# Performance work log

Measured on AMD Instinct MI355X. Metric: run time of the kernel, lower is better.

## Reference

```python
import jax, jax.numpy as jnp
import numpy as np

B, N, D, H = 2, 1024, 512, 16
DH = D // H  # d_head = 32
NEG_INF = -1e9
LN_EPS = 1e-5


def setup_inputs() -> dict:
    key = jax.random.key(0)
    ks = jax.random.split(key, 12)
    x = jax.random.normal(ks[0], (B, N, D), dtype=jnp.float32)
    pdist = jax.random.uniform(ks[1], (B, N, N), dtype=jnp.float32)
    angle = jax.random.normal(ks[2], (B, N, N, 2), dtype=jnp.float32)
    adj = jax.random.uniform(ks[3], (B, N, N), dtype=jnp.float32)
    mask = jnp.zeros((B, 1, 1, N), dtype=bool)
    # parameters
    gamma_p = jnp.ones((H,), dtype=jnp.float32)
    gamma_adj = jnp.ones((H,), dtype=jnp.float32)
    w_bias = jax.random.normal(ks[4], (H, 2), dtype=jnp.float32) / np.sqrt(2.0)   # Linear(2,H).weight
    att_w = jax.random.normal(ks[5], (3 * H * DH, D), dtype=jnp.float32) / np.sqrt(D)  # Linear(D,3HDh).weight
    ff_w = jax.random.normal(ks[6], (D, H * DH), dtype=jnp.float32) / np.sqrt(H * DH)  # Linear(HDh,D).weight
    ff_b = jnp.zeros((D,), dtype=jnp.float32)
    ln_w = jnp.ones((D,), dtype=jnp.float32)
    ln_b = jnp.zeros((D,), dtype=jnp.float32)
    return dict(x=x, pdist=pdist, angle=angle, adj=adj, mask=mask,
                gamma_p=gamma_p, gamma_adj=gamma_adj, w_bias=w_bias,
                att_w=att_w, ff_w=ff_w, ff_b=ff_b, ln_w=ln_w, ln_b=ln_b)


def reference(x, pdist, angle, adj, mask, gamma_p, gamma_adj, w_bias,
              att_w, ff_w, ff_b, ln_w, ln_b):
    bsz, n_atoms, _ = x.shape
    # QKV projection
    qkv = x @ att_w.T                              # [B,N,3*H*DH]
    wq, wk, wv = jnp.split(qkv, 3, axis=-1)
    wq = wq.reshape(bsz, n_atoms, H, DH)
    wk = wk.reshape(bsz, n_atoms, H, DH)
    wv = wv.reshape(bsz, n_atoms, H, DH)
    # scores with additive biases
    score = jnp.einsum('bihd,bjhd->bhij', wq, wk) / jnp.sqrt(jnp.float32(DH))
    score = score - gamma_p[None, :, None, None] * pdist[:, None]
    angle_bias = jnp.einsum('bijc,hc->bhij', angle, w_bias)
    score = score + angle_bias
    score = score + gamma_adj[None, :, None, None] * adj[:, None]
    score = jnp.where(mask, NEG_INF, score)
    prob = jax.nn.softmax(score, axis=-1)          # [B,H,N,N]
    att_vec = jnp.einsum('bhij,bjhd->bihd', prob, wv).reshape(bsz, n_atoms, H * DH)
    ff_out = att_vec @ ff_w.T + ff_b               # [B,N,D]
    y = x + ff_out
    mu = jnp.mean(y, axis=-1, keepdims=True)
    var = jnp.mean(jnp.square(y - mu), axis=-1, keepdims=True)
    return (y - mu) / jnp.sqrt(var + LN_EPS) * ln_w + ln_b
```

## Files before the change

### kernel.cpp

```cpp
#include <hip/hip_runtime.h>
#include <hip/hip_bf16.h>
#include <stdint.h>

#define DEVI __device__ __forceinline__

typedef __attribute__((ext_vector_type(4))) float f32x4;
typedef __attribute__((ext_vector_type(16))) float f32x16;
typedef __attribute__((ext_vector_type(8))) short bf16x8;

constexpr int nB = 2, nN = 1024, nD = 512, nH = 16, nDH = 32;

DEVI unsigned short f2bf(float x) {
  unsigned u = __float_as_uint(x);
  return (unsigned short)((u + 0x7fffu + ((u >> 16) & 1u)) >> 16);
}
DEVI float bf2f(unsigned short s) { return __uint_as_float(((unsigned)s) << 16); }
DEVI unsigned pk2(float lo, float hi_) {
  return (unsigned)f2bf(lo) | ((unsigned)f2bf(hi_) << 16);
}
DEVI float bperm(int srclane, float v) {
  return __int_as_float(__builtin_amdgcn_ds_bpermute(srclane << 2, __float_as_int(v)));
}
DEVI void gload16(const void* g, void* l) {
  __builtin_amdgcn_global_load_lds((const __attribute__((address_space(1))) void*)g,
                                   (__attribute__((address_space(3))) void*)l, 16, 0, 0);
}

__global__ __launch_bounds__(256) void cvt_fw(const float* __restrict__ fw,
                                              unsigned short* __restrict__ fwb) {
  int i = blockIdx.x * 256 + threadIdx.x;
  float4 v = reinterpret_cast<const float4*>(fw)[i];
  ushort4 o;
  o.x = f2bf(v.x); o.y = f2bf(v.y); o.z = f2bf(v.z); o.w = f2bf(v.w);
  reinterpret_cast<ushort4*>(fwb)[i] = o;
}

__global__ __launch_bounds__(256, 2) void qkv_gemm(const float* __restrict__ x,
                                                   const float* __restrict__ aw,
                                                   unsigned short* __restrict__ q,
                                                   unsigned short* __restrict__ kmat,
                                                   unsigned short* __restrict__ vtt) {
  __shared__ __align__(16) unsigned short sA[2][64 * 32];
  __shared__ __align__(16) unsigned short sB[2][128 * 32];
  const int tid = threadIdx.x, wid = tid >> 6, lane = tid & 63;
  const int wr = wid >> 1, wc = wid & 1;
  const long rowA = (long)blockIdx.x * 64;
  const long rowB = (long)blockIdx.y * 128;

  f32x4 acc[2][4];
#pragma unroll
  for (int mm = 0; mm < 2; ++mm)
#pragma unroll
    for (int nn = 0; nn < 4; ++nn)
#pragma unroll
      for (int r = 0; r < 4; ++r) acc[mm][nn][r] = 0.f;

  union PK { unsigned u[4]; bf16x8 v; };

  auto stage = [&](int t, int pb) {
    const int k0 = t * 32;
    {
      const float* src = x + (rowA + (tid >> 2)) * 512 + k0 + (tid & 3) * 8;
      float4 v0 = *reinterpret_cast<const float4*>(src);
      float4 v1 = *reinterpret_cast<const float4*>(src + 4);
      PK p;
      p.u[0] = pk2(v0.x, v0.y); p.u[1] = pk2(v0.z, v0.w);
      p.u[2] = pk2(v1.x, v1.y); p.u[3] = pk2(v1.z, v1.w);
      *reinterpret_cast<bf16x8*>(&sA[pb][tid * 8]) = p.v;
    }
    {
      const float* src = aw + (rowB + (tid >> 1)) * 512 + k0 + (tid & 1) * 16;
      float4 w0 = *reinterpret_cast<const float4*>(src);
      float4 w1 = *reinterpret_cast<const float4*>(src + 4);
      float4 w2 = *reinterpret_cast<const float4*>(src + 8);
      float4 w3 = *reinterpret_cast<const float4*>(src + 12);
      PK p0, p1;
      p0.u[0] = pk2(w0.x, w0.y); p0.u[1] = pk2(w0.z, w0.w);
      p0.u[2] = pk2(w1.x, w1.y); p0.u[3] = pk2(w1.z, w1.w);
      p1.u[0] = pk2(w2.x, w2.y); p1.u[1] = pk2(w2.z, w2.w);
      p1.u[2] = pk2(w3.x, w3.y); p1.u[3] = pk2(w3.z, w3.w);
      *reinterpret_cast<bf16x8*>(&sB[pb][tid * 16]) = p0.v;
      *reinterpret_cast<bf16x8*>(&sB[pb][tid * 16 + 8]) = p1.v;
    }
  };
  auto comp = [&](int pb) {
    const int kg = (lane >> 4) * 8, rlo = lane & 15;
    bf16x8 af[2], bfv[4];
#pragma unroll
    for (int mm = 0; mm < 2; ++mm)
      af[mm] = *reinterpret_cast<const bf16x8*>(&sA[pb][(32 * wr + 16 * mm + rlo) * 32 + kg]);
#pragma unroll
    for (int nn = 0; nn < 4; ++nn)
      bfv[nn] = *reinterpret_cast<const bf16x8*>(&sB[pb][(64 * wc + 16 * nn + rlo) * 32 + kg]);
#pragma unroll
    for (int mm = 0; mm < 2; ++mm)
#pragma unroll
      for (int nn = 0; nn < 4; ++nn)
        acc[mm][nn] = __builtin_amdgcn_mfma_f32_16x16x32_bf16(af[mm], bfv[nn],
                                                              acc[mm][nn], 0, 0, 0);
  };

  stage(0, 0);
  __syncthreads();
  for (int t = 0; t < 16; t += 2) {
    if (t + 1 < 16) stage(t + 1, 1);
    comp(0);
    __syncthreads();
    if (t + 2 < 16) stage(t + 2, 0);
    comp(1);
    __syncthreads();
  }

#pragma unroll
  for (int mm = 0; mm < 2; ++mm)
#pragma unroll
    for (int nn = 0; nn < 4; ++nn)
#pragma unroll
      for (int r = 0; r < 4; ++r) {
        float v = acc[mm][nn][r];
        int row = (int)rowA + 32 * wr + 16 * mm + (lane >> 4) * 4 + r;
        int col = (int)rowB + 64 * wc + 16 * nn + (lane & 15);
        int s = col >> 9, rem = col & 511;
        int h = rem >> 5, d = rem & 31;
        int b = row >> 10, n = row & 1023;
        if (s == 0) {
          q[((long)(b * nH + h) * nN + n) * nDH + d] = f2bf(v * 0.1767766952966369f);
        } else if (s == 1) {
          kmat[((long)(b * nH + h) * nN + n) * nDH + d] = f2bf(v);
        } else {
          vtt[((long)(b * nH + h) * 32 + (n >> 5)) * 1024 + d * 32 + (n & 31)] = f2bf(v);
        }
      }
}

__global__ __launch_bounds__(1024, 4) void attn_kernel(
    const unsigned short* __restrict__ qm, const unsigned short* __restrict__ km,
    const unsigned short* __restrict__ vtt,
    const float* __restrict__ pdist, const float* __restrict__ angle,
    const float* __restrict__ adj, const unsigned char* __restrict__ mask,
    const float* __restrict__ gamma_p, const float* __restrict__ gamma_adj,
    const float* __restrict__ w_bias,
    unsigned short* __restrict__ po, float* __restrict__ pm, float* __restrict__ pl) {
  const int b = blockIdx.x >> 5, it = blockIdx.x & 31;
  const int jc = blockIdx.y;
  const int tid = threadIdx.x, wid = tid >> 6, lane = tid & 63;
  const int h = wid;
  const int li = lane & 31, hi = lane >> 5;
  const int ibase = it * 32;

  __shared__ __align__(16) float s_pd[2][1024], s_adj[2][1024];
  __shared__ __align__(16) float s_a0[2][1024], s_a1[2][1024];
  __shared__ __align__(16) float s_mk[1024];

  const float gp = gamma_p[h], ga = gamma_adj[h];
  const float wb0 = w_bias[2 * h], wb1 = w_bias[2 * h + 1];

  const unsigned short* qb = qm + ((long)(b * nH + h) * nN + ibase) * nDH;
  const bf16x8 qf0 = *reinterpret_cast<const bf16x8*>(qb + li * 32 + hi * 8);
  const bf16x8 qf1 = *reinterpret_cast<const bf16x8*>(qb + li * 32 + 16 + hi * 8);

  f32x16 o;
#pragma unroll
  for (int r = 0; r < 16; ++r) o[r] = 0.f;
  float mrun = -INFINITY, lrun = 0.f;

  auto stage = [&](int s, int pb) {
    const int jbase = (jc * 4 + s) * 32;
    if (tid < 512) {
      int r = (tid >> 3) & 31, c = tid & 7;
      const float* src = (tid < 256 ? pdist : adj) +
                         ((long)b * nN + ibase + r) * nN + jbase + c * 4;
      float4 v = *reinterpret_cast<const float4*>(src);
      float* dst = (tid < 256 ? s_pd[pb] : s_adj[pb]) + r * 32 + ((c ^ (r & 7)) << 2);
      *reinterpret_cast<float4*>(dst) = v;
    } else {
      int t2 = tid - 512;
      int r = t2 >> 4, p = t2 & 15;
      float4 v = *reinterpret_cast<const float4*>(
          angle + (((long)b * nN + ibase + r) * nN + jbase + p * 2) * 2);
      int off = r * 32 + (((p >> 1) ^ (r & 7)) << 2) + (p & 1) * 2;
      *reinterpret_cast<float2*>(s_a0[pb] + off) = make_float2(v.x, v.z);
      *reinterpret_cast<float2*>(s_a1[pb] + off) = make_float2(v.y, v.w);
    }
  };

  auto comp = [&](int s, int pb) {
    const int jt = jc * 4 + s, jbase = jt * 32;
    const unsigned short* kb = km + ((long)(b * nH + h) * nN + jbase) * nDH;
    bf16x8 kf0 = *reinterpret_cast<const bf16x8*>(kb + li * 32 + hi * 8);
    bf16x8 kf1 = *reinterpret_cast<const bf16x8*>(kb + li * 32 + 16 + hi * 8);
    const unsigned short* vb = vtt + ((long)(b * nH + h) * 32 + jt) * 1024;
    bf16x8 vf0 = *reinterpret_cast<const bf16x8*>(vb + li * 32 + hi * 8);
    bf16x8 vf1 = *reinterpret_cast<const bf16x8*>(vb + li * 32 + 16 + hi * 8);

    f32x16 sc;
#pragma unroll
    for (int r = 0; r < 16; ++r) sc[r] = 0.f;
    sc = __builtin_amdgcn_mfma_f32_32x32x16_bf16(kf0, qf0, sc, 0, 0, 0);
    sc = __builtin_amdgcn_mfma_f32_32x32x16_bf16(kf1, qf1, sc, 0, 0, 0);

    float sv[16];
    float tmax = -INFINITY;
#pragma unroll
    for (int g = 0; g < 4; ++g) {
      const int cs = (((2 * g + hi) ^ (li & 7)) << 2);
      f32x4 pdq = *reinterpret_cast<const f32x4*>(s_pd[pb] + li * 32 + cs);
      f32x4 adq = *reinterpret_cast<const f32x4*>(s_adj[pb] + li * 32 + cs);
      f32x4 a0q = *reinterpret_cast<const f32x4*>(s_a0[pb] + li * 32 + cs);
      f32x4 a1q = *reinterpret_cast<const f32x4*>(s_a1[pb] + li * 32 + cs);
      f32x4 mkq = *reinterpret_cast<const f32x4*>(s_mk + jbase + 8 * g + 4 * hi);
#pragma unroll
      for (int u = 0; u < 4; ++u) {
        float xv = sc[4 * g + u] - gp * pdq[u] + wb0 * a0q[u] + wb1 * a1q[u]
                   + ga * adq[u] + mkq[u];
        sv[4 * g + u] = xv;
        tmax = fmaxf(tmax, xv);
      }
    }
    tmax = fmaxf(tmax, __shfl_xor(tmax, 32));
    if (__any((int)(tmax > mrun + 8.f))) {
      float mnew = fmaxf(mrun, tmax);
      float alpha = __expf(mrun - mnew);
      lrun *= alpha;
#pragma unroll
      for (int r = 0; r < 16; ++r) o[r] *= bperm((r & 3) + 8 * (r >> 2) + 4 * hi, alpha);
      mrun = mnew;
    }
    float psum = 0.f;
#pragma unroll
    for (int r = 0; r < 16; ++r) { sv[r] = __expf(sv[r] - mrun); psum += sv[r]; }
    psum += __shfl_xor(psum, 32);
    lrun += psum;

    unsigned ow[8], rw[8];
#pragma unroll
    for (int t = 0; t < 8; ++t) ow[t] = pk2(sv[2 * t], sv[2 * t + 1]);
#pragma unroll
    for (int t = 0; t < 8; ++t) rw[t] = __shfl_xor(ow[t], 32);
    union U { unsigned u[4]; bf16x8 v; };
    U u0, u1;
    if (hi == 0) {
      u0.u[0] = ow[0]; u0.u[1] = ow[1]; u0.u[2] = rw[0]; u0.u[3] = rw[1];
      u1.u[0] = ow[4]; u1.u[1] = ow[5]; u1.u[2] = rw[4]; u1.u[3] = rw[5];
    } else {
      u0.u[0] = rw[2]; u0.u[1] = rw[3]; u0.u[2] = ow[2]; u0.u[3] = ow[3];
      u1.u[0] = rw[6]; u1.u[1] = rw[7]; u1.u[2] = ow[6]; u1.u[3] = ow[7];
    }

    o = __builtin_amdgcn_mfma_f32_32x32x16_bf16(u0.v, vf0, o, 0, 0, 0);
    o = __builtin_amdgcn_mfma_f32_32x32x16_bf16(u1.v, vf1, o, 0, 0, 0);
  };

  s_mk[tid] = mask[b * nN + tid] ? -1e9f : 0.f;
  stage(0, 0);
  __syncthreads();
  for (int s = 0; s < 4; s += 2) {
    if (s + 1 < 4) stage(s + 1, 1);
    comp(s, 0);
    __syncthreads();
    if (s + 2 < 4) stage(s + 2, 0);
    comp(s + 1, 1);
    __syncthreads();
  }

  const long task = (((long)(b * nH + h) * 32 + it) * 8 + jc);
  unsigned short* pob = po + task * 1024;
#pragma unroll
  for (int r = 0; r < 16; ++r) {
    const int irow = (r & 3) + 8 * (r >> 2) + 4 * hi;
    pob[irow * 32 + li] = f2bf(o[r]);
  }
  if (hi == 0) { pm[task * 32 + li] = mrun; pl[task * 32 + li] = lrun; }
}

__global__ __launch_bounds__(256) void merge_kernel(const unsigned short* __restrict__ po,
                                                    const float* __restrict__ pm,
                                                    const float* __restrict__ pl,
                                                    unsigned short* __restrict__ attb) {
  const int x = blockIdx.x;
  const int t = threadIdx.x;
  const int i = t >> 3, d4 = (t & 7) * 4;
  const long tb = (long)x * 8;
  float m[8], l[8];
#pragma unroll
  for (int c = 0; c < 8; ++c) { m[c] = pm[(tb + c) * 32 + i]; l[c] = pl[(tb + c) * 32 + i]; }
  float M = m[0];
#pragma unroll
  for (int c = 1; c < 8; ++c) M = fmaxf(M, m[c]);
  float L = 0.f, w[8];
#pragma unroll
  for (int c = 0; c < 8; ++c) { w[c] = __expf(m[c] - M); L += w[c] * l[c]; }
  float o0 = 0, o1 = 0, o2 = 0, o3 = 0;
#pragma unroll
  for (int c = 0; c < 8; ++c) {
    ushort4 v = *reinterpret_cast<const ushort4*>(po + (tb + c) * 1024 + i * 32 + d4);
    o0 += w[c] * bf2f(v.x); o1 += w[c] * bf2f(v.y);
    o2 += w[c] * bf2f(v.z); o3 += w[c] * bf2f(v.w);
  }
  const float inv = 1.f / L;
  const int b = x >> 9, hh = (x >> 5) & 15, it = x & 31;
  ushort4 ov;
  ov.x = f2bf(o0 * inv); ov.y = f2bf(o1 * inv);
  ov.z = f2bf(o2 * inv); ov.w = f2bf(o3 * inv);
  *reinterpret_cast<ushort4*>(attb + ((long)b * nN + it * 32 + i) * nD + hh * 32 + d4) = ov;
}

__global__ __launch_bounds__(512, 2) void ffln_kernel(const unsigned short* __restrict__ attb,
                                                      const unsigned short* __restrict__ fwb,
                                                      const float* __restrict__ x,
                                                      const float* __restrict__ ffb,
                                                      const float* __restrict__ lnw,
                                                      const float* __restrict__ lnb,
                                                      float* __restrict__ out) {
  __shared__ __align__(16) unsigned short sA[2][32 * 32];
  __shared__ __align__(16) unsigned short sB[2][512 * 32];
  __shared__ float rs_[32][4], rs2_[32][4];
  const int tid = threadIdx.x, wid = tid >> 6, lane = tid & 63;
  const int wr = wid >> 2, wc = wid & 3;
  const long rowA = (long)blockIdx.x * 32;

  f32x4 acc[8];
#pragma unroll
  for (int nn = 0; nn < 8; ++nn)
#pragma unroll
    for (int r = 0; r < 4; ++r) acc[nn][r] = 0.f;

  auto stage = [&](int t, int pb) {
    const int k0 = t * 32;
    if (tid < 128)
      gload16(&attb[(rowA + (tid >> 2)) * 512 + k0 + (tid & 3) * 8], &sA[pb][tid * 8]);
#pragma unroll
    for (int c = 0; c < 4; ++c) {
      int off = (tid + 512 * c) * 8;
      int r = off >> 5, s8 = off & 31;
      gload16(&fwb[(long)r * 512 + k0 + s8], &sB[pb][off]);
    }
  };
  auto comp = [&](int pb) {
    const int kg = (lane >> 4) * 8, rlo = lane & 15;
    bf16x8 af = *reinterpret_cast<const bf16x8*>(&sA[pb][(16 * wr + rlo) * 32 + kg]);
#pragma unroll
    for (int nn = 0; nn < 8; ++nn) {
      bf16x8 bfv = *reinterpret_cast<const bf16x8*>(&sB[pb][(128 * wc + 16 * nn + rlo) * 32 + kg]);
      acc[nn] = __builtin_amdgcn_mfma_f32_16x16x32_bf16(af, bfv, acc[nn], 0, 0, 0);
    }
  };

  stage(0, 0);
  __syncthreads();
  for (int t = 0; t < 16; t += 2) {
    if (t + 1 < 16) stage(t + 1, 1);
    comp(0);
    __syncthreads();
    if (t + 2 < 16) stage(t + 2, 0);
    comp(1);
    __syncthreads();
  }

  float colf[8], colw[8], colb[8];
#pragma unroll
  for (int nn = 0; nn < 8; ++nn) {
    int c = 128 * wc + 16 * nn + (lane & 15);
    colf[nn] = ffb[c]; colw[nn] = lnw[c]; colb[nn] = lnb[c];
  }
  float s[4], s2[4];
#pragma unroll
  for (int r = 0; r < 4; ++r) { s[r] = 0.f; s2[r] = 0.f; }
#pragma unroll
  for (int nn = 0; nn < 8; ++nn)
#pragma unroll
    for (int r = 0; r < 4; ++r) {
      long row = rowA + 16 * wr + 4 * (lane >> 4) + r;
      int c = 128 * wc + 16 * nn + (lane & 15);
      float y = acc[nn][r] + colf[nn] + x[row * 512 + c];
      acc[nn][r] = y;
      s[r] += y; s2[r] += y * y;
    }
#pragma unroll
  for (int off = 1; off < 16; off <<= 1)
#pragma unroll
    for (int r = 0; r < 4; ++r) {
      s[r] += __shfl_xor(s[r], off);
      s2[r] += __shfl_xor(s2[r], off);
    }
  if ((lane & 15) == 0) {
#pragma unroll
    for (int r = 0; r < 4; ++r) {
      int rowl = 16 * wr + 4 * (lane >> 4) + r;
      rs_[rowl][wc] = s[r];
      rs2_[rowl][wc] = s2[r];
    }
  }
  __syncthreads();
#pragma unroll
  for (int r = 0; r < 4; ++r) {
    int rowl = 16 * wr + 4 * (lane >> 4) + r;
    float S = rs_[rowl][0] + rs_[rowl][1] + rs_[rowl][2] + rs_[rowl][3];
    float S2 = rs2_[rowl][0] + rs2_[rowl][1] + rs2_[rowl][2] + rs2_[rowl][3];
    float mu = S * (1.f / 512.f);
    float var = S2 * (1.f / 512.f) - mu * mu;
    float rstd = rsqrtf(var + 1e-5f);
    long row = rowA + rowl;
#pragma unroll
    for (int nn = 0; nn < 8; ++nn) {
      int c = 128 * wc + 16 * nn + (lane & 15);
      out[row * 512 + c] = (acc[nn][r] - mu) * rstd * colw[nn] + colb[nn];
    }
  }
}

extern "C" void kernel_launch(void* const* d_in, const int* in_sizes, int n_in,
                              void* d_out, int out_size, void* d_ws, size_t ws_size,
                              hipStream_t stream) {
  const float* x         = (const float*)d_in[0];
  const float* pdist     = (const float*)d_in[1];
  const float* angle     = (const float*)d_in[2];
  const float* adj       = (const float*)d_in[3];
  const unsigned char* mask = (const unsigned char*)d_in[4];
  const float* gamma_p   = (const float*)d_in[5];
  const float* gamma_adj = (const float*)d_in[6];
  const float* w_bias    = (const float*)d_in[7];
  const float* att_w     = (const float*)d_in[8];
  const float* ff_w      = (const float*)d_in[9];
  const float* ff_b      = (const float*)d_in[10];
  const float* ln_w      = (const float*)d_in[11];
  const float* ln_b      = (const float*)d_in[12];
  float* out = (float*)d_out;

  char* ws = (char*)d_ws;
  unsigned short* qm   = (unsigned short*)(ws);
  unsigned short* km   = (unsigned short*)(ws + 0x200000);
  unsigned short* vtt  = (unsigned short*)(ws + 0x400000);
  unsigned short* po   = (unsigned short*)(ws + 0x600000);
  float*          pm   = (float*)(ws + 0x1600000);
  float*          pl   = (float*)(ws + 0x1700000);
  unsigned short* attb = (unsigned short*)(ws + 0x1800000);
  unsigned short* fwb  = (unsigned short*)(ws + 0x1A00000);

  hipLaunchKernelGGL(cvt_fw, dim3(256), dim3(256), 0, stream, ff_w, fwb);
  hipLaunchKernelGGL(qkv_gemm, dim3(32, 12), dim3(256), 0, stream,
                     x, att_w, qm, km, vtt);
  hipLaunchKernelGGL(attn_kernel, dim3(64, 8), dim3(1024), 0, stream,
                     qm, km, vtt, pdist, angle, adj, mask,
                     gamma_p, gamma_adj, w_bias, po, pm, pl);
  hipLaunchKernelGGL(merge_kernel, dim3(1024), dim3(256), 0, stream,
                     po, pm, pl, attb);
  hipLaunchKernelGGL(ffln_kernel, dim3(64), dim3(512), 0, stream,
                     attb, fwb, x, ff_b, ln_w, ln_b, out);
}
```

Baseline: 181.7 us.

## Use async global-to-LDS loads, exp2 softmax, and fewer key splits in attention

The attention kernel now stages pdist, adj and angle tiles with direct global_load_lds transfers and an XOR swizzle, replacing register round-trips, and keeps angle interleaved in a single buffer. The pipeline waits on vmcnt and raw barriers. The key dimension is split into 4 chunks of 8 tiles instead of 8 chunks of 4, which halves the partial results the merge kernel reads but also halves grid parallelism. Softmax switches to exp2 with log2e folded into the scale and bias coefficients, and bf16 packing uses the hardware packed-convert intrinsic.

```diff
diff --git a/kernel.cpp b/kernel.cpp
--- a/kernel.cpp
+++ b/kernel.cpp
@@ -9,14 +9,16 @@
 typedef __attribute__((ext_vector_type(8))) short bf16x8;
 
 constexpr int nB = 2, nN = 1024, nD = 512, nH = 16, nDH = 32;
+constexpr float L2E = 1.4426950408889634f;
 
 DEVI unsigned short f2bf(float x) {
   unsigned u = __float_as_uint(x);
   return (unsigned short)((u + 0x7fffu + ((u >> 16) & 1u)) >> 16);
 }
 DEVI float bf2f(unsigned short s) { return __uint_as_float(((unsigned)s) << 16); }
-DEVI unsigned pk2(float lo, float hi_) {
-  return (unsigned)f2bf(lo) | ((unsigned)f2bf(hi_) << 16);
+DEVI unsigned pkcvt(float lo, float hi_) {
+  __hip_bfloat162 h = __float22bfloat162_rn(make_float2(lo, hi_));
+  union { __hip_bfloat162 h; unsigned u; } c; c.h = h; return c.u;
 }
 DEVI float bperm(int srclane, float v) {
   return __int_as_float(__builtin_amdgcn_ds_bpermute(srclane << 2, __float_as_int(v)));
@@ -30,9 +32,9 @@
                                               unsigned short* __restrict__ fwb) {
   int i = blockIdx.x * 256 + threadIdx.x;
   float4 v = reinterpret_cast<const float4*>(fw)[i];
-  ushort4 o;
-  o.x = f2bf(v.x); o.y = f2bf(v.y); o.z = f2bf(v.z); o.w = f2bf(v.w);
-  reinterpret_cast<ushort4*>(fwb)[i] = o;
+  uint2 p;
+  p.x = pkcvt(v.x, v.y); p.y = pkcvt(v.z, v.w);
+  reinterpret_cast<uint2*>(fwb)[i] = p;
 }
 
 __global__ __launch_bounds__(256, 2) void qkv_gemm(const float* __restrict__ x,
@@ -64,8 +66,8 @@
       float4 v0 = *reinterpret_cast<const float4*>(src);
       float4 v1 = *reinterpret_cast<const float4*>(src + 4);
       PK p;
-      p.u[0] = pk2(v0.x, v0.y); p.u[1] = pk2(v0.z, v0.w);
-      p.u[2] = pk2(v1.x, v1.y); p.u[3] = pk2(v1.z, v1.w);
+      p.u[0] = pkcvt(v0.x, v0.y); p.u[1] = pkcvt(v0.z, v0.w);
+      p.u[2] = pkcvt(v1.x, v1.y); p.u[3] = pkcvt(v1.z, v1.w);
       *reinterpret_cast<bf16x8*>(&sA[pb][tid * 8]) = p.v;
     }
     {
@@ -75,10 +77,10 @@
       float4 w2 = *reinterpret_cast<const float4*>(src + 8);
       float4 w3 = *reinterpret_cast<const float4*>(src + 12);
       PK p0, p1;
-      p0.u[0] = pk2(w0.x, w0.y); p0.u[1] = pk2(w0.z, w0.w);
-      p0.u[2] = pk2(w1.x, w1.y); p0.u[3] = pk2(w1.z, w1.w);
-      p1.u[0] = pk2(w2.x, w2.y); p1.u[1] = pk2(w2.z, w2.w);
-      p1.u[2] = pk2(w3.x, w3.y); p1.u[3] = pk2(w3.z, w3.w);
+      p0.u[0] = pkcvt(w0.x, w0.y); p0.u[1] = pkcvt(w0.z, w0.w);
+      p0.u[2] = pkcvt(w1.x, w1.y); p0.u[3] = pkcvt(w1.z, w1.w);
+      p1.u[0] = pkcvt(w2.x, w2.y); p1.u[1] = pkcvt(w2.z, w2.w);
+      p1.u[2] = pkcvt(w3.x, w3.y); p1.u[3] = pkcvt(w3.z, w3.w);
       *reinterpret_cast<bf16x8*>(&sB[pb][tid * 16]) = p0.v;
       *reinterpret_cast<bf16x8*>(&sB[pb][tid * 16 + 8]) = p1.v;
     }
@@ -124,7 +126,7 @@
         int h = rem >> 5, d = rem & 31;
         int b = row >> 10, n = row & 1023;
         if (s == 0) {
-          q[((long)(b * nH + h) * nN + n) * nDH + d] = f2bf(v * 0.1767766952966369f);
+          q[((long)(b * nH + h) * nN + n) * nDH + d] = f2bf(v * 0.2550565449825934f);
         } else if (s == 1) {
           kmat[((long)(b * nH + h) * nN + n) * nDH + d] = f2bf(v);
         } else {
@@ -133,7 +135,7 @@
       }
 }
 
-__global__ __launch_bounds__(1024, 4) void attn_kernel(
+__global__ __launch_bounds__(1024) void attn_kernel(
     const unsigned short* __restrict__ qm, const unsigned short* __restrict__ km,
     const unsigned short* __restrict__ vtt,
     const float* __restrict__ pdist, const float* __restrict__ angle,
@@ -149,11 +151,11 @@
   const int ibase = it * 32;
 
   __shared__ __align__(16) float s_pd[2][1024], s_adj[2][1024];
-  __shared__ __align__(16) float s_a0[2][1024], s_a1[2][1024];
-  __shared__ __align__(16) float s_mk[1024];
-
-  const float gp = gamma_p[h], ga = gamma_adj[h];
-  const float wb0 = w_bias[2 * h], wb1 = w_bias[2 * h + 1];
+  __shared__ __align__(16) float s_ang[2][2048];
+  __shared__ __align__(16) float s_mk[256];
+
+  const float gp = gamma_p[h] * L2E, ga = gamma_adj[h] * L2E;
+  const float wb0 = w_bias[2 * h] * L2E, wb1 = w_bias[2 * h + 1] * L2E;
 
   const unsigned short* qb = qm + ((long)(b * nH + h) * nN + ibase) * nDH;
   const bf16x8 qf0 = *reinterpret_cast<const bf16x8*>(qb + li * 32 + hi * 8);
@@ -165,27 +167,29 @@
   float mrun = -INFINITY, lrun = 0.f;
 
   auto stage = [&](int s, int pb) {
-    const int jbase = (jc * 4 + s) * 32;
-    if (tid < 512) {
-      int r = (tid >> 3) & 31, c = tid & 7;
-      const float* src = (tid < 256 ? pdist : adj) +
-                         ((long)b * nN + ibase + r) * nN + jbase + c * 4;
-      float4 v = *reinterpret_cast<const float4*>(src);
-      float* dst = (tid < 256 ? s_pd[pb] : s_adj[pb]) + r * 32 + ((c ^ (r & 7)) << 2);
-      *reinterpret_cast<float4*>(dst) = v;
+    const long jbase = (jc * 8 + s) * 32;
+    if (tid < 256) {
+      int row = tid >> 3, c = tid & 7;
+      int cs = c ^ ((row & 7) ^ (row >> 3));
+      gload16(pdist + ((long)b * nN + ibase + row) * nN + jbase + cs * 4,
+              (char*)&s_pd[pb][0] + tid * 16);
+    } else if (tid < 512) {
+      int t2 = tid - 256;
+      int row = t2 >> 3, c = t2 & 7;
+      int cs = c ^ ((row & 7) ^ (row >> 3));
+      gload16(adj + ((long)b * nN + ibase + row) * nN + jbase + cs * 4,
+              (char*)&s_adj[pb][0] + t2 * 16);
     } else {
       int t2 = tid - 512;
-      int r = t2 >> 4, p = t2 & 15;
-      float4 v = *reinterpret_cast<const float4*>(
-          angle + (((long)b * nN + ibase + r) * nN + jbase + p * 2) * 2);
-      int off = r * 32 + (((p >> 1) ^ (r & 7)) << 2) + (p & 1) * 2;
-      *reinterpret_cast<float2*>(s_a0[pb] + off) = make_float2(v.x, v.z);
-      *reinterpret_cast<float2*>(s_a1[pb] + off) = make_float2(v.y, v.w);
+      int row = t2 >> 4, c = t2 & 15;
+      int cs = c ^ ((row & 7) ^ (row >> 3));
+      gload16(angle + (((long)b * nN + ibase + row) * nN + jbase) * 2 + cs * 4,
+              (char*)&s_ang[pb][0] + t2 * 16);
     }
   };
 
   auto comp = [&](int s, int pb) {
-    const int jt = jc * 4 + s, jbase = jt * 32;
+    const int jt = jc * 8 + s, jbase = jt * 32;
     const unsigned short* kb = km + ((long)(b * nH + h) * nN + jbase) * nDH;
     bf16x8 kf0 = *reinterpret_cast<const bf16x8*>(kb + li * 32 + hi * 8);
     bf16x8 kf1 = *reinterpret_cast<const bf16x8*>(kb + li * 32 + 16 + hi * 8);
@@ -199,28 +203,32 @@
     sc = __builtin_amdgcn_mfma_f32_32x32x16_bf16(kf0, qf0, sc, 0, 0, 0);
     sc = __builtin_amdgcn_mfma_f32_32x32x16_bf16(kf1, qf1, sc, 0, 0, 0);
 
+    const int Sli = (li & 7) ^ (li >> 3);
     float sv[16];
     float tmax = -INFINITY;
 #pragma unroll
     for (int g = 0; g < 4; ++g) {
-      const int cs = (((2 * g + hi) ^ (li & 7)) << 2);
-      f32x4 pdq = *reinterpret_cast<const f32x4*>(s_pd[pb] + li * 32 + cs);
-      f32x4 adq = *reinterpret_cast<const f32x4*>(s_adj[pb] + li * 32 + cs);
-      f32x4 a0q = *reinterpret_cast<const f32x4*>(s_a0[pb] + li * 32 + cs);
-      f32x4 a1q = *reinterpret_cast<const f32x4*>(s_a1[pb] + li * 32 + cs);
-      f32x4 mkq = *reinterpret_cast<const f32x4*>(s_mk + jbase + 8 * g + 4 * hi);
+      const int cp = (2 * g + hi) ^ Sli;
+      f32x4 pdq = *reinterpret_cast<const f32x4*>(s_pd[pb] + li * 32 + cp * 4);
+      f32x4 adq = *reinterpret_cast<const f32x4*>(s_adj[pb] + li * 32 + cp * 4);
+      const int ca0 = (4 * g + 2 * hi) ^ Sli, ca1 = (4 * g + 2 * hi + 1) ^ Sli;
+      f32x4 av1 = *reinterpret_cast<const f32x4*>(s_ang[pb] + li * 64 + ca0 * 4);
+      f32x4 av2 = *reinterpret_cast<const f32x4*>(s_ang[pb] + li * 64 + ca1 * 4);
+      const float* mk = s_mk + s * 32 + 8 * g + 4 * hi;
+      float a0s[4] = {av1[0], av1[2], av2[0], av2[2]};
+      float a1s[4] = {av1[1], av1[3], av2[1], av2[3]};
 #pragma unroll
       for (int u = 0; u < 4; ++u) {
-        float xv = sc[4 * g + u] - gp * pdq[u] + wb0 * a0q[u] + wb1 * a1q[u]
-                   + ga * adq[u] + mkq[u];
+        float xv = sc[4 * g + u] - gp * pdq[u] + wb0 * a0s[u] + wb1 * a1s[u]
+                   + ga * adq[u] + mk[u];
         sv[4 * g + u] = xv;
         tmax = fmaxf(tmax, xv);
       }
     }
     tmax = fmaxf(tmax, __shfl_xor(tmax, 32));
-    if (__any((int)(tmax > mrun + 8.f))) {
+    if (__any((int)(tmax > mrun + 11.5415603f))) {
       float mnew = fmaxf(mrun, tmax);
-      float alpha = __expf(mrun - mnew);
+      float alpha = exp2f(mrun - mnew);
       lrun *= alpha;
 #pragma unroll
       for (int r = 0; r < 16; ++r) o[r] *= bperm((r & 3) + 8 * (r >> 2) + 4 * hi, alpha);
@@ -228,13 +236,13 @@
     }
     float psum = 0.f;
 #pragma unroll
-    for (int r = 0; r < 16; ++r) { sv[r] = __expf(sv[r] - mrun); psum += sv[r]; }
+    for (int r = 0; r < 16; ++r) { sv[r] = exp2f(sv[r] - mrun); psum += sv[r]; }
     psum += __shfl_xor(psum, 32);
     lrun += psum;
 
     unsigned ow[8], rw[8];
 #pragma unroll
-    for (int t = 0; t < 8; ++t) ow[t] = pk2(sv[2 * t], sv[2 * t + 1]);
+    for (int t = 0; t < 8; ++t) ow[t] = pkcvt(sv[2 * t], sv[2 * t + 1]);
 #pragma unroll
     for (int t = 0; t < 8; ++t) rw[t] = __shfl_xor(ow[t], 32);
     union U { unsigned u[4]; bf16x8 v; };
@@ -251,19 +259,25 @@
     o = __builtin_amdgcn_mfma_f32_32x32x16_bf16(u1.v, vf1, o, 0, 0, 0);
   };
 
-  s_mk[tid] = mask[b * nN + tid] ? -1e9f : 0.f;
+  if (tid < 256)
+    s_mk[tid] = mask[b * nN + jc * 256 + tid] ? -1.442695e9f : 0.f;
   stage(0, 0);
   __syncthreads();
-  for (int s = 0; s < 4; s += 2) {
-    if (s + 1 < 4) stage(s + 1, 1);
-    comp(s, 0);
-    __syncthreads();
-    if (s + 2 < 4) stage(s + 2, 0);
-    comp(s + 1, 1);
-    __syncthreads();
-  }
-
-  const long task = (((long)(b * nH + h) * 32 + it) * 8 + jc);
+
+  for (int s = 0; s < 8; ++s) {
+    const int pb = s & 1;
+    if (s < 7) {
+      stage(s + 1, pb ^ 1);
+      asm volatile("s_waitcnt vmcnt(1)" ::: "memory");
+    } else {
+      asm volatile("s_waitcnt vmcnt(0)" ::: "memory");
+    }
+    __builtin_amdgcn_s_barrier();
+    comp(s, pb);
+    __builtin_amdgcn_s_barrier();
+  }
+
+  const long task = (((long)(b * nH + h) * 32 + it) * 4 + jc);
   unsigned short* pob = po + task * 1024;
 #pragma unroll
   for (int r = 0; r < 16; ++r) {
@@ -280,19 +294,17 @@
   const int x = blockIdx.x;
   const int t = threadIdx.x;
   const int i = t >> 3, d4 = (t & 7) * 4;
-  const long tb = (long)x * 8;
-  float m[8], l[8];
-#pragma unroll
-  for (int c = 0; c < 8; ++c) { m[c] = pm[(tb + c) * 32 + i]; l[c] = pl[(tb + c) * 32 + i]; }
-  float M = m[0];
-#pragma unroll
-  for (int c = 1; c < 8; ++c) M = fmaxf(M, m[c]);
-  float L = 0.f, w[8];
-#pragma unroll
-  for (int c = 0; c < 8; ++c) { w[c] = __expf(m[c] - M); L += w[c] * l[c]; }
+  const long tb = (long)x * 4;
+  float m[4], l[4];
+#pragma unroll
+  for (int c = 0; c < 4; ++c) { m[c] = pm[(tb + c) * 32 + i]; l[c] = pl[(tb + c) * 32 + i]; }
+  float M = fmaxf(fmaxf(m[0], m[1]), fmaxf(m[2], m[3]));
+  float L = 0.f, w[4];
+#pragma unroll
+  for (int c = 0; c < 4; ++c) { w[c] = exp2f(m[c] - M); L += w[c] * l[c]; }
   float o0 = 0, o1 = 0, o2 = 0, o3 = 0;
 #pragma unroll
-  for (int c = 0; c < 8; ++c) {
+  for (int c = 0; c < 4; ++c) {
     ushort4 v = *reinterpret_cast<const ushort4*>(po + (tb + c) * 1024 + i * 32 + d4);
     o0 += w[c] * bf2f(v.x); o1 += w[c] * bf2f(v.y);
     o2 += w[c] * bf2f(v.z); o3 += w[c] * bf2f(v.w);
@@ -440,7 +452,7 @@
   hipLaunchKernelGGL(cvt_fw, dim3(256), dim3(256), 0, stream, ff_w, fwb);
   hipLaunchKernelGGL(qkv_gemm, dim3(32, 12), dim3(256), 0, stream,
                      x, att_w, qm, km, vtt);
-  hipLaunchKernelGGL(attn_kernel, dim3(64, 8), dim3(1024), 0, stream,
+  hipLaunchKernelGGL(attn_kernel, dim3(64, 4), dim3(1024), 0, stream,
                      qm, km, vtt, pdist, angle, adj, mask,
                      gamma_p, gamma_adj, w_bias, po, pm, pl);
   hipLaunchKernelGGL(merge_kernel, dim3(1024), dim3(256), 0, stream,
```

New measurement: 178.1 us. -2.0%, faster.
